# Performance work log

Hardware: AMD Instinct MI355X
Metric: run time of the kernel (lower is better)

Reference implementation:

```python
import jax, jax.numpy as jnp
import numpy as np

B, S, D, H, T = 64, 256, 256, 512, 48
EPS = 1e-5  # BatchNorm1d default eps


def setup_inputs():
    key = jax.random.key(0)
    ks = jax.random.split(key, 40)
    rn = lambda k, sh, s=0.05: jax.random.normal(k, sh, dtype=jnp.float32) * s
    inp = {}
    inp["inputs"] = jax.random.normal(ks[0], (B, S, D), dtype=jnp.float32)
    inp["tags"] = jax.random.randint(ks[1], (B, S), 0, T)
    i = 2
    for l, din in ((0, D), (1, 2 * H)):
        for d in ("f", "b"):
            inp["Wih_l%d%s" % (l, d)] = rn(ks[i], (4 * H, din)); i += 1
            inp["Whh_l%d%s" % (l, d)] = rn(ks[i], (4 * H, H)); i += 1
            inp["bih_l%d%s" % (l, d)] = rn(ks[i], (4 * H,)); i += 1
            inp["bhh_l%d%s" % (l, d)] = rn(ks[i], (4 * H,)); i += 1
    inp["bn_gamma"] = jnp.ones((2 * H,), jnp.float32)
    inp["bn_beta"] = jnp.zeros((2 * H,), jnp.float32)
    inp["bn_mean"] = rn(ks[i], (2 * H,)); i += 1
    inp["bn_var"] = jax.random.uniform(ks[i], (2 * H,), jnp.float32, 0.5, 1.5); i += 1
    inp["fc1_w"] = rn(ks[i], (H, 2 * H)); i += 1
    inp["fc1_b"] = rn(ks[i], (H,)); i += 1
    inp["fc2_w"] = rn(ks[i], (H // 2, H)); i += 1
    inp["fc2_b"] = rn(ks[i], (H // 2,)); i += 1
    inp["fc3_w"] = rn(ks[i], (T, H // 2)); i += 1
    inp["fc3_b"] = rn(ks[i], (T,)); i += 1
    inp["crf_start"] = rn(ks[i], (T,), 0.1); i += 1
    inp["crf_end"] = rn(ks[i], (T,), 0.1); i += 1
    inp["crf_trans"] = rn(ks[i], (T, T), 0.1); i += 1
    return inp


def _lstm_dir(x, Wih, Whh, bih, bhh, reverse):
    # x: [B,S,Din] -> hs: [B,S,H]; PyTorch gate order i,f,g,o
    xs = jnp.swapaxes(x, 0, 1)  # [S,B,Din]
    if reverse:
        xs = xs[::-1]
    pre = xs @ Wih.T + bih  # [S,B,4H] input projection precomputed
    h0 = jnp.zeros((x.shape[0], Whh.shape[1]), x.dtype)

    def step(carry, p):
        h, c = carry
        g = p + h @ Whh.T + bhh
        i, f, gg, o = jnp.split(g, 4, axis=-1)
        c = jax.nn.sigmoid(f) * c + jax.nn.sigmoid(i) * jnp.tanh(gg)
        h = jax.nn.sigmoid(o) * jnp.tanh(c)
        return (h, c), h

    _, hs = jax.lax.scan(step, (h0, h0), pre)
    if reverse:
        hs = hs[::-1]
    return jnp.swapaxes(hs, 0, 1)


def _model(inputs, tags, Wih_l0f, Whh_l0f, bih_l0f, bhh_l0f,
           Wih_l0b, Whh_l0b, bih_l0b, bhh_l0b,
           Wih_l1f, Whh_l1f, bih_l1f, bhh_l1f,
           Wih_l1b, Whh_l1b, bih_l1b, bhh_l1b,
           bn_gamma, bn_beta, bn_mean, bn_var,
           fc1_w, fc1_b, fc2_w, fc2_b, fc3_w, fc3_b,
           crf_start, crf_end, crf_trans):
    # 2-layer bidirectional LSTM
    x = jnp.concatenate([_lstm_dir(inputs, Wih_l0f, Whh_l0f, bih_l0f, bhh_l0f, False),
                         _lstm_dir(inputs, Wih_l0b, Whh_l0b, bih_l0b, bhh_l0b, True)], -1)
    x = jnp.concatenate([_lstm_dir(x, Wih_l1f, Whh_l1f, bih_l1f, bhh_l1f, False),
                         _lstm_dir(x, Wih_l1b, Whh_l1b, bih_l1b, bhh_l1b, True)], -1)
    # dropout: identity in eval; BatchNorm1d over channel dim, eval (running stats)
    x = (x - bn_mean) * (bn_gamma / jnp.sqrt(bn_var + EPS)) + bn_beta
    x = jax.nn.relu(x @ fc1_w.T + fc1_b)
    x = jax.nn.relu(x @ fc2_w.T + fc2_b)
    em = x @ fc3_w.T + fc3_b  # [B,S,T] emissions

    # CRF negative log-likelihood, full mask, reduction='mean'
    em_tag = jnp.take_along_axis(em, tags[..., None], axis=2)[..., 0]  # [B,S]
    num = (crf_start[tags[:, 0]] + em_tag.sum(1)
           + crf_trans[tags[:, :-1], tags[:, 1:]].sum(1)
           + crf_end[tags[:, -1]])

    et = jnp.swapaxes(em, 0, 1)  # [S,B,T]

    def step(alpha, e_t):
        # alpha: [B,T]; e_t: [B,T]
        alpha = jax.nn.logsumexp(alpha[:, :, None] + crf_trans[None], axis=1) + e_t
        return alpha, None

    alpha, _ = jax.lax.scan(step, crf_start + et[0], et[1:])
    logZ = jax.nn.logsumexp(alpha + crf_end, axis=1)
    return -jnp.mean(num - logZ)


def reference(inputs, tags, Wih_l0f, Whh_l0f, bih_l0f, bhh_l0f,
              Wih_l0b, Whh_l0b, bih_l0b, bhh_l0b,
              Wih_l1f, Whh_l1f, bih_l1f, bhh_l1f,
              Wih_l1b, Whh_l1b, bih_l1b, bhh_l1b,
              bn_gamma, bn_beta, bn_mean, bn_var,
              fc1_w, fc1_b, fc2_w, fc2_b, fc3_w, fc3_b,
              crf_start, crf_end, crf_trans):
    return _model(inputs, tags, Wih_l0f, Whh_l0f, bih_l0f, bhh_l0f,
                  Wih_l0b, Whh_l0b, bih_l0b, bhh_l0b,
                  Wih_l1f, Whh_l1f, bih_l1f, bhh_l1f,
                  Wih_l1b, Whh_l1b, bih_l1b, bhh_l1b,
                  bn_gamma, bn_beta, bn_mean, bn_var,
                  fc1_w, fc1_b, fc2_w, fc2_b, fc3_w, fc3_b,
                  crf_start, crf_end, crf_trans)
```

## Files before the change

kernel.cpp:

```cpp
#include <hip/hip_runtime.h>
#include <hip/hip_bf16.h>
#include <math.h>

#define Bz 64
#define Sz 256
#define Dz 256
#define Hz 512
#define FH 2048
#define OH 1024
#define Tz 48
#define EPSV 1e-5f
#define LOG2E 1.44269504f

typedef __hip_bfloat16 bf16;
typedef __attribute__((ext_vector_type(8))) short short8;
typedef __attribute__((ext_vector_type(4))) float floatx4;
typedef unsigned long long u64;

__device__ __forceinline__ float b2f(bf16 v){ return __bfloat162float(v); }
__device__ __forceinline__ float fsig(float x){
  float e = __builtin_amdgcn_exp2f(-x*LOG2E);
  return __builtin_amdgcn_rcpf(1.f + e);
}
__device__ __forceinline__ float ftanh(float x){
  float e = __builtin_amdgcn_exp2f(x*(2.f*LOG2E));
  return 1.f - 2.f*__builtin_amdgcn_rcpf(e + 1.f);
}

__device__ __forceinline__ void load4f(const bf16* p, float v[4]) {
  ushort4 t = *(const ushort4*)p;
  v[0] = __uint_as_float(((unsigned)t.x) << 16);
  v[1] = __uint_as_float(((unsigned)t.y) << 16);
  v[2] = __uint_as_float(((unsigned)t.z) << 16);
  v[3] = __uint_as_float(((unsigned)t.w) << 16);
}
__device__ __forceinline__ void storev(float* p, float v){ *p = v; }
__device__ __forceinline__ void storev(bf16* p, float v){ *p = __float2bfloat16(v); }

__global__ __launch_bounds__(256) void castf2b(const float* __restrict__ in, bf16* __restrict__ out, int n)
{
  int i = (blockIdx.x*256 + threadIdx.x)*4;
  if (i >= n) return;
  float4 v = *(const float4*)(in + i);
  bf16 tmp[4];
  tmp[0] = __float2bfloat16(v.x); tmp[1] = __float2bfloat16(v.y);
  tmp[2] = __float2bfloat16(v.z); tmp[3] = __float2bfloat16(v.w);
  *(uint2*)(out + i) = *(const uint2*)tmp;
}

__global__ __launch_bounds__(256) void bnprep_k(const float* __restrict__ gamma, const float* __restrict__ beta,
  const float* __restrict__ mean, const float* __restrict__ var,
  float* __restrict__ scale, float* __restrict__ shift)
{
  int i = blockIdx.x*256 + threadIdx.x;
  if (i >= OH) return;
  float s = gamma[i]*rsqrtf(var[i]+EPSV);
  scale[i] = s; shift[i] = beta[i] - mean[i]*s;
}

template<typename TC>
__global__ __launch_bounds__(256) void gemm_mfma(
  const bf16* __restrict__ A, const bf16* __restrict__ W,
  const float* __restrict__ b1, const float* __restrict__ b2,
  TC* __restrict__ Cv, int M, int N, int K, int relu)
{
  __shared__ bf16 As[128][40];
  __shared__ bf16 Bs[128][40];
  int tid = threadIdx.x;
  int wave = tid>>6, lane = tid&63, l15 = lane&15, quad = lane>>4;
  int m0 = blockIdx.y*128, n0 = blockIdx.x*128;
  int wm = (wave>>1)*64, wn = (wave&1)*64;
  int srow = tid>>1, scw = (tid&1)*16;
  const bf16* Ap = A + (size_t)(m0+srow)*K + scw;
  const bf16* Wp = W + (size_t)(n0+srow)*K + scw;
  floatx4 zero = {0.f,0.f,0.f,0.f};
  floatx4 acc[4][4];
  #pragma unroll
  for (int i=0;i<4;i++)
    #pragma unroll
    for (int j=0;j<4;j++) acc[i][j] = zero;

  for (int k0 = 0; k0 < K; k0 += 32) {
    float4 a0 = *(const float4*)Ap, a1 = *(const float4*)(Ap+8);
    float4 w0 = *(const float4*)Wp, w1 = *(const float4*)(Wp+8);
    Ap += 32; Wp += 32;
    __syncthreads();
    *(float4*)&As[srow][scw]   = a0; *(float4*)&As[srow][scw+8] = a1;
    *(float4*)&Bs[srow][scw]   = w0; *(float4*)&Bs[srow][scw+8] = w1;
    __syncthreads();
    short8 af[4], bfv[4];
    #pragma unroll
    for (int mi=0;mi<4;mi++) af[mi]  = *(const short8*)&As[wm+mi*16+l15][quad*8];
    #pragma unroll
    for (int ni=0;ni<4;ni++) bfv[ni] = *(const short8*)&Bs[wn+ni*16+l15][quad*8];
    #pragma unroll
    for (int mi=0;mi<4;mi++)
      #pragma unroll
      for (int ni=0;ni<4;ni++)
        acc[mi][ni] = __builtin_amdgcn_mfma_f32_16x16x32_bf16(af[mi], bfv[ni], acc[mi][ni], 0,0,0);
  }
  #pragma unroll
  for (int mi=0;mi<4;mi++){
    #pragma unroll
    for (int ni=0;ni<4;ni++){
      int n = n0 + wn + ni*16 + l15;
      float bb = (b1 ? b1[n] : 0.f) + (b2 ? b2[n] : 0.f);
      #pragma unroll
      for (int r=0;r<4;r++){
        int m = m0 + wm + mi*16 + quad*4 + r;
        float v = acc[mi][ni][r] + bb;
        if (relu) v = fmaxf(v, 0.f);
        storev(&Cv[(size_t)m*N + n], v);
      }
    }
  }
}

__global__ __launch_bounds__(256) void gemm_nt_small(
  const bf16* __restrict__ A, const float* __restrict__ W,
  const float* __restrict__ b1, float* __restrict__ Cv, int M, int N, int K)
{
  __shared__ float As[8][128];
  __shared__ float Ws[8][128];
  int tid = threadIdx.x;
  int tx = tid & 15, ty = tid >> 4;
  int m0 = blockIdx.y * 128, n0 = blockIdx.x * 128;
  int sr = tid >> 1;
  int sk = (tid & 1) * 4;
  const bf16* Ap = A + (size_t)(m0 + sr) * K + sk;
  bool wok = (n0 + sr) < N;
  const float* Wp = W + (size_t)(wok ? (n0 + sr) : 0) * K + sk;
  float acc[8][8] = {};
  for (int k0 = 0; k0 < K; k0 += 8) {
    float av[4], wv[4];
    load4f(Ap, av);
    if (wok) { float4 t = *(const float4*)Wp; wv[0]=t.x; wv[1]=t.y; wv[2]=t.z; wv[3]=t.w; }
    else { wv[0]=wv[1]=wv[2]=wv[3]=0.f; }
    Ap += 8; Wp += 8;
    __syncthreads();
    As[sk+0][sr]=av[0]; As[sk+1][sr]=av[1]; As[sk+2][sr]=av[2]; As[sk+3][sr]=av[3];
    Ws[sk+0][sr]=wv[0]; Ws[sk+1][sr]=wv[1]; Ws[sk+2][sr]=wv[2]; Ws[sk+3][sr]=wv[3];
    __syncthreads();
    #pragma unroll
    for (int kk = 0; kk < 8; kk++) {
      float a[8], w[8];
      *(float4*)&a[0] = *(const float4*)&As[kk][ty*8];
      *(float4*)&a[4] = *(const float4*)&As[kk][ty*8+4];
      *(float4*)&w[0] = *(const float4*)&Ws[kk][tx*8];
      *(float4*)&w[4] = *(const float4*)&Ws[kk][tx*8+4];
      #pragma unroll
      for (int i=0;i<8;i++)
        #pragma unroll
        for (int j=0;j<8;j++) acc[i][j] += a[i]*w[j];
    }
  }
  #pragma unroll
  for (int i=0;i<8;i++){
    int m = m0 + ty*8 + i;
    #pragma unroll
    for (int j=0;j<8;j++){
      int n = n0 + tx*8 + j;
      if (n < N) Cv[(size_t)m*N + n] = acc[i][j] + b1[n];
    }
  }
}

__global__ __launch_bounds__(256,1) void lstm_persist(
  const bf16* __restrict__ preF, const bf16* __restrict__ preB,
  const bf16* __restrict__ WF, const bf16* __restrict__ WB,
  bf16* __restrict__ hbuf,
  bf16* __restrict__ xout,
  const float* __restrict__ bnscale, const float* __restrict__ bnshift,
  int* __restrict__ cnt)
{
  __shared__ bf16 wlds[64][520];
  int blk = blockIdx.x;
  int dir = blk & 1;
  int js  = blk >> 1;
  int j0  = js * 16;
  const bf16* pre = dir ? preB : preF;
  const bf16* W   = dir ? WB : WF;
  int colOff = dir ? Hz : 0;
  int tid = threadIdx.x;
  int wave = tid >> 6, lane = tid & 63, l15 = lane & 15, quad = lane >> 4;
  int* myc = cnt + dir*256;

  for (int chunk = tid; chunk < 64*64; chunk += 256) {
    int n = chunk >> 6, col = (chunk & 63) * 8;
    int g = n >> 4, idx = n & 15;
    *(float4*)&wlds[n][col] = *(const float4*)(W + ((size_t)(g*512 + j0 + idx))*Hz + col);
  }
  __syncthreads();

  int bb = wave*16 + quad*4;
  int j  = j0 + l15;
  float sc = bnscale ? bnscale[colOff + j] : 1.f;
  float sh = bnshift ? bnshift[colOff + j] : 0.f;
  int useBN = bnscale ? 1 : 0;
  float c[4] = {0.f,0.f,0.f,0.f};

  float pg[4][4];
  {
    int t0 = dir ? (Sz-1) : 0;
    #pragma unroll
    for (int r=0;r<4;r++){
      const bf16* pb = pre + ((size_t)(bb+r)*Sz + t0)*FH;
      #pragma unroll
      for (int g=0;g<4;g++) pg[g][r] = b2f(pb[g*512 + j]);
    }
  }

  for (int t = 0; t < Sz; t++) {
    int tcur = dir ? (Sz-1-t) : t;
    floatx4 zero = {0.f,0.f,0.f,0.f};
    floatx4 acc[4] = {zero, zero, zero, zero};

    short8 af[16];
    if (t > 0) {
      const bf16* hprev = hbuf + ((size_t)((t&1)*2 + dir))*Bz*Hz;
      #pragma unroll
      for (int ks=0;ks<16;ks++){
        const u64* hp = (const u64*)(hprev + (size_t)(wave*16 + l15)*Hz + ks*32 + quad*8);
        union { u64 q[2]; short8 v; } uu;
        uu.q[0] = __hip_atomic_load(hp,     __ATOMIC_RELAXED, __HIP_MEMORY_SCOPE_SYSTEM);
        uu.q[1] = __hip_atomic_load(hp + 1, __ATOMIC_RELAXED, __HIP_MEMORY_SCOPE_SYSTEM);
        af[ks] = uu.v;
      }
    }

    float pgn[4][4];
    if (t+1 < Sz) {
      int tnext = dir ? (Sz-2-t) : (t+1);
      #pragma unroll
      for (int r=0;r<4;r++){
        const bf16* pb = pre + ((size_t)(bb+r)*Sz + tnext)*FH;
        #pragma unroll
        for (int g=0;g<4;g++) pgn[g][r] = b2f(pb[g*512 + j]);
      }
    }

    if (t > 0) {
      #pragma unroll
      for (int g=0; g<4; g++)
        #pragma unroll
        for (int ks=0; ks<16; ks++){
          short8 bfv = *(const short8*)&wlds[g*16 + l15][ks*32 + quad*8];
          acc[g] = __builtin_amdgcn_mfma_f32_16x16x32_bf16(af[ks], bfv, acc[g], 0,0,0);
        }
    }

    bf16* hnext = hbuf + ((size_t)(((t+1)&1)*2 + dir))*Bz*Hz;
    float hval[4];
    #pragma unroll
    for (int r=0;r<4;r++){
      int b = bb + r;
      float gi = acc[0][r] + pg[0][r];
      float gf = acc[1][r] + pg[1][r];
      float gg = acc[2][r] + pg[2][r];
      float go = acc[3][r] + pg[3][r];
      float cv = fsig(gf)*c[r] + fsig(gi)*ftanh(gg);
      float h  = fsig(go)*ftanh(cv);
      c[r] = cv;
      hval[r] = h;
      bf16 hb = __float2bfloat16(h);
      union { bf16 b16; short s; } u; u.b16 = hb;
      __hip_atomic_store((short*)(hnext + (size_t)b*Hz + j), u.s,
                         __ATOMIC_RELAXED, __HIP_MEMORY_SCOPE_SYSTEM);
    }

    if (t < Sz-1) {
      __syncthreads();
      if (tid == 0)
        __hip_atomic_fetch_add(&myc[t], 1, __ATOMIC_RELAXED, __HIP_MEMORY_SCOPE_SYSTEM);

      #pragma unroll
      for (int r=0;r<4;r++){
        float xv = useBN ? (hval[r]*sc + sh) : hval[r];
        xout[((size_t)(bb+r)*Sz + tcur)*OH + colOff + j] = __float2bfloat16(xv);
      }

      while (__hip_atomic_load(&myc[t], __ATOMIC_RELAXED, __HIP_MEMORY_SCOPE_SYSTEM) < 32) {}
      asm volatile("" ::: "memory");

      #pragma unroll
      for (int g=0;g<4;g++)
        #pragma unroll
        for (int r=0;r<4;r++) pg[g][r] = pgn[g][r];
    } else {
      #pragma unroll
      for (int r=0;r<4;r++){
        float xv = useBN ? (hval[r]*sc + sh) : hval[r];
        xout[((size_t)(bb+r)*Sz + tcur)*OH + colOff + j] = __float2bfloat16(xv);
      }
    }
  }
}

__global__ __launch_bounds__(64) void crf_k(const float* __restrict__ em, const int* __restrict__ tags,
  const float* __restrict__ start, const float* __restrict__ endv, const float* __restrict__ trans,
  float* __restrict__ result)
{
  __shared__ float tr[Tz*Tz];
  __shared__ float alpha[2][Tz];
  int b = blockIdx.x, tid = threadIdx.x;
  for (int i = tid; i < Tz*Tz; i += 64) tr[i] = trans[i];
  float np = 0.f;
  for (int t = tid; t < Sz; t += 64) {
    int tg = tags[b*Sz + t];
    np += em[((size_t)b*Sz + t)*Tz + tg];
    if (t+1 < Sz) np += trans[tg*Tz + tags[b*Sz + t + 1]];
  }
  #pragma unroll
  for (int off = 32; off; off >>= 1) np += __shfl_down(np, off);
  float num = 0.f;
  if (tid == 0) num = np + start[tags[b*Sz]] + endv[tags[b*Sz + Sz-1]];
  if (tid < Tz) alpha[0][tid] = start[tid] + em[((size_t)b*Sz)*Tz + tid];
  __syncthreads();
  int cur = 0;
  for (int t = 1; t < Sz; t++) {
    if (tid < Tz) {
      float m = -1e30f;
      for (int i = 0; i < Tz; i++) m = fmaxf(m, alpha[cur][i] + tr[i*Tz + tid]);
      float sum = 0.f;
      for (int i = 0; i < Tz; i++) sum += expf(alpha[cur][i] + tr[i*Tz + tid] - m);
      alpha[1-cur][tid] = m + logf(sum) + em[((size_t)b*Sz + t)*Tz + tid];
    }
    cur ^= 1;
    __syncthreads();
  }
  float a = (tid < Tz) ? alpha[cur][tid] + endv[tid] : -1e30f;
  float m = a;
  #pragma unroll
  for (int off = 32; off; off >>= 1) m = fmaxf(m, __shfl_down(m, off));
  m = __shfl(m, 0);
  float e = (tid < Tz) ? expf(a - m) : 0.f;
  #pragma unroll
  for (int off = 32; off; off >>= 1) e += __shfl_down(e, off);
  if (tid == 0) result[b] = num - (m + logf(e));
}

__global__ __launch_bounds__(64) void finalize_k(const float* __restrict__ result, float* __restrict__ outp)
{
  float v = result[threadIdx.x];
  #pragma unroll
  for (int off = 32; off; off >>= 1) v += __shfl_down(v, off);
  if (threadIdx.x == 0) outp[0] = -(v * (1.f/64.f));
}

extern "C" void kernel_launch(void* const* d_in, const int* in_sizes, int n_in,
                              void* d_out, int out_size, void* d_ws, size_t ws_size,
                              hipStream_t stream)
{
  (void)in_sizes; (void)n_in; (void)out_size; (void)ws_size;
  const float* inputs = (const float*)d_in[0];
  const int*   tags   = (const int*)d_in[1];
  const float* Wih[2][2] = {{(const float*)d_in[2],  (const float*)d_in[6]},
                            {(const float*)d_in[10], (const float*)d_in[14]}};
  const float* Whh[2][2] = {{(const float*)d_in[3],  (const float*)d_in[7]},
                            {(const float*)d_in[11], (const float*)d_in[15]}};
  const float* bih[2][2] = {{(const float*)d_in[4],  (const float*)d_in[8]},
                            {(const float*)d_in[12], (const float*)d_in[16]}};
  const float* bhh[2][2] = {{(const float*)d_in[5],  (const float*)d_in[9]},
                            {(const float*)d_in[13], (const float*)d_in[17]}};
  const float* bn_gamma = (const float*)d_in[18];
  const float* bn_beta  = (const float*)d_in[19];
  const float* bn_mean  = (const float*)d_in[20];
  const float* bn_var   = (const float*)d_in[21];
  const float* fc1_w = (const float*)d_in[22];
  const float* fc1_b = (const float*)d_in[23];
  const float* fc2_w = (const float*)d_in[24];
  const float* fc2_b = (const float*)d_in[25];
  const float* fc3_w = (const float*)d_in[26];
  const float* fc3_b = (const float*)d_in[27];
  const float* crf_start = (const float*)d_in[28];
  const float* crf_end   = (const float*)d_in[29];
  const float* crf_trans = (const float*)d_in[30];

  const size_t M = (size_t)Bz*Sz;
  char* p = (char*)d_ws;
  auto alloc = [&](size_t bytes) { char* r = p; p += (bytes + 255) & ~(size_t)255; return r; };
  bf16*  preF  = (bf16*) alloc(M*FH*sizeof(bf16));
  bf16*  preB  = (bf16*) alloc(M*FH*sizeof(bf16));
  bf16*  xbuf  = (bf16*) alloc(M*OH*sizeof(bf16));
  bf16*  inbf  = (bf16*) alloc(M*Dz*sizeof(bf16));
  bf16*  Wih0A = (bf16*) alloc((size_t)FH*Dz*sizeof(bf16));
  bf16*  Wih0B = (bf16*) alloc((size_t)FH*Dz*sizeof(bf16));
  bf16*  Wih1A = (bf16*) alloc((size_t)FH*OH*sizeof(bf16));
  bf16*  Wih1B = (bf16*) alloc((size_t)FH*OH*sizeof(bf16));
  bf16*  Whh0A = (bf16*) alloc((size_t)FH*Hz*sizeof(bf16));
  bf16*  Whh0B = (bf16*) alloc((size_t)FH*Hz*sizeof(bf16));
  bf16*  Whh1A = (bf16*) alloc((size_t)FH*Hz*sizeof(bf16));
  bf16*  Whh1B = (bf16*) alloc((size_t)FH*Hz*sizeof(bf16));
  bf16*  fc1wb = (bf16*) alloc((size_t)Hz*OH*sizeof(bf16));
  bf16*  fc2wb = (bf16*) alloc((size_t)256*Hz*sizeof(bf16));
  bf16*  hbuf  = (bf16*) alloc(4*(size_t)Bz*Hz*sizeof(bf16));
  int*   cnt   = (int*)  alloc(1024*sizeof(int));
  float* bnscale = (float*)alloc(OH*sizeof(float));
  float* bnshift = (float*)alloc(OH*sizeof(float));
  float* result  = (float*)alloc(Bz*sizeof(float));
  float* em   = (float*)inbf;
  bf16* fc1o = (bf16*)preF;
  bf16* fc2o = (bf16*)preB;

  dim3 tb(256);
  auto cast = [&](const float* src, bf16* dst, size_t n){
    castf2b<<<(n/4 + 255)/256, tb, 0, stream>>>(src, dst, (int)n);
  };

  hipMemsetAsync(cnt, 0, 1024*sizeof(int), stream);
  cast(inputs, inbf, M*Dz);
  cast(Wih[0][0], Wih0A, (size_t)FH*Dz);
  cast(Wih[0][1], Wih0B, (size_t)FH*Dz);
  cast(Wih[1][0], Wih1A, (size_t)FH*OH);
  cast(Wih[1][1], Wih1B, (size_t)FH*OH);
  cast(Whh[0][0], Whh0A, (size_t)FH*Hz);
  cast(Whh[0][1], Whh0B, (size_t)FH*Hz);
  cast(Whh[1][0], Whh1A, (size_t)FH*Hz);
  cast(Whh[1][1], Whh1B, (size_t)FH*Hz);
  cast(fc1_w, fc1wb, (size_t)Hz*OH);
  cast(fc2_w, fc2wb, (size_t)256*Hz);
  bnprep_k<<<OH/256, tb, 0, stream>>>(bn_gamma, bn_beta, bn_mean, bn_var, bnscale, bnshift);

  gemm_mfma<bf16><<<dim3(FH/128, M/128), tb, 0, stream>>>(inbf, Wih0A, bih[0][0], bhh[0][0], preF, M, FH, Dz, 0);
  gemm_mfma<bf16><<<dim3(FH/128, M/128), tb, 0, stream>>>(inbf, Wih0B, bih[0][1], bhh[0][1], preB, M, FH, Dz, 0);
  lstm_persist<<<64, tb, 0, stream>>>(preF, preB, Whh0A, Whh0B, hbuf, xbuf, nullptr, nullptr, cnt);
  gemm_mfma<bf16><<<dim3(FH/128, M/128), tb, 0, stream>>>(xbuf, Wih1A, bih[1][0], bhh[1][0], preF, M, FH, OH, 0);
  gemm_mfma<bf16><<<dim3(FH/128, M/128), tb, 0, stream>>>(xbuf, Wih1B, bih[1][1], bhh[1][1], preB, M, FH, OH, 0);
  lstm_persist<<<64, tb, 0, stream>>>(preF, preB, Whh1A, Whh1B, hbuf, xbuf, bnscale, bnshift, cnt + 512);
  gemm_mfma<bf16><<<dim3(Hz/128, M/128), tb, 0, stream>>>(xbuf, fc1wb, fc1_b, nullptr, fc1o, M, Hz, OH, 1);
  gemm_mfma<bf16><<<dim3(256/128, M/128), tb, 0, stream>>>(fc1o, fc2wb, fc2_b, nullptr, fc2o, M, 256, Hz, 1);
  gemm_nt_small<<<dim3(1, M/128), tb, 0, stream>>>(fc2o, fc3_w, fc3_b, em, M, Tz, 256);
  crf_k<<<Bz, 64, 0, stream>>>(em, tags, crf_start, crf_end, crf_trans, result);
  finalize_k<<<1, 64, 0, stream>>>(result, (float*)d_out);
}
```

Baseline: 4.417 ms.

## Replace atomic-counter grid barrier with per-block stamps and aggregator blocks

Each step's barrier in the persistent LSTM changes from 32 blocks doing atomic fetch-add on one counter per timestep to each block storing its own timestep stamp. Two extra aggregator blocks, one per direction, poll the 32 stamps with a wave-wide any test and publish an epoch value that the worker blocks spin on. This is meant to remove contention from atomic read-modify-writes on a shared counter and shorten the barrier latency on the sequential critical path. It adds an extra hop through the aggregator and depends on all 66 blocks being resident at the same time.

Result: slower. 4.685 ms (+6.1%).

```diff
diff --git a/kernel.cpp b/kernel.cpp
--- a/kernel.cpp
+++ b/kernel.cpp
@@ -171,10 +171,29 @@
   bf16* __restrict__ hbuf,
   bf16* __restrict__ xout,
   const float* __restrict__ bnscale, const float* __restrict__ bnshift,
-  int* __restrict__ cnt)
-{
+  int* __restrict__ flags)
+{
+  int blk = blockIdx.x;
+
+  if (blk >= 64) {
+    int dir = blk - 64;
+    if (threadIdx.x < 32) {
+      int* st = flags + dir*32;
+      int* ep = flags + 128 + dir*64;
+      int lane = threadIdx.x;
+      for (int t = 0; t < Sz-1; t++) {
+        int v;
+        do {
+          v = __hip_atomic_load(&st[lane], __ATOMIC_RELAXED, __HIP_MEMORY_SCOPE_SYSTEM);
+        } while (__any(v <= t));
+        if (lane == 0)
+          __hip_atomic_store(ep, t+1, __ATOMIC_RELAXED, __HIP_MEMORY_SCOPE_SYSTEM);
+      }
+    }
+    return;
+  }
+
   __shared__ bf16 wlds[64][520];
-  int blk = blockIdx.x;
   int dir = blk & 1;
   int js  = blk >> 1;
   int j0  = js * 16;
@@ -183,7 +202,8 @@
   int colOff = dir ? Hz : 0;
   int tid = threadIdx.x;
   int wave = tid >> 6, lane = tid & 63, l15 = lane & 15, quad = lane >> 4;
-  int* myc = cnt + dir*256;
+  int* mystamp = flags + dir*32 + js;
+  int* ep      = flags + 128 + dir*64;
 
   for (int chunk = tid; chunk < 64*64; chunk += 256) {
     int n = chunk >> 6, col = (chunk & 63) * 8;
@@ -271,7 +291,7 @@
     if (t < Sz-1) {
       __syncthreads();
       if (tid == 0)
-        __hip_atomic_fetch_add(&myc[t], 1, __ATOMIC_RELAXED, __HIP_MEMORY_SCOPE_SYSTEM);
+        __hip_atomic_store(mystamp, t+1, __ATOMIC_RELAXED, __HIP_MEMORY_SCOPE_SYSTEM);
 
       #pragma unroll
       for (int r=0;r<4;r++){
@@ -279,7 +299,7 @@
         xout[((size_t)(bb+r)*Sz + tcur)*OH + colOff + j] = __float2bfloat16(xv);
       }
 
-      while (__hip_atomic_load(&myc[t], __ATOMIC_RELAXED, __HIP_MEMORY_SCOPE_SYSTEM) < 32) {}
+      while (__hip_atomic_load(ep, __ATOMIC_RELAXED, __HIP_MEMORY_SCOPE_SYSTEM) <= t) {}
       asm volatile("" ::: "memory");
 
       #pragma unroll
@@ -394,7 +414,7 @@
   bf16*  fc1wb = (bf16*) alloc((size_t)Hz*OH*sizeof(bf16));
   bf16*  fc2wb = (bf16*) alloc((size_t)256*Hz*sizeof(bf16));
   bf16*  hbuf  = (bf16*) alloc(4*(size_t)Bz*Hz*sizeof(bf16));
-  int*   cnt   = (int*)  alloc(1024*sizeof(int));
+  int*   flags = (int*)  alloc(512*sizeof(int));
   float* bnscale = (float*)alloc(OH*sizeof(float));
   float* bnshift = (float*)alloc(OH*sizeof(float));
   float* result  = (float*)alloc(Bz*sizeof(float));
@@ -407,7 +427,7 @@
     castf2b<<<(n/4 + 255)/256, tb, 0, stream>>>(src, dst, (int)n);
   };
 
-  hipMemsetAsync(cnt, 0, 1024*sizeof(int), stream);
+  hipMemsetAsync(flags, 0, 512*sizeof(int), stream);
   cast(inputs, inbf, M*Dz);
   cast(Wih[0][0], Wih0A, (size_t)FH*Dz);
   cast(Wih[0][1], Wih0B, (size_t)FH*Dz);
@@ -423,10 +443,10 @@
 
   gemm_mfma<bf16><<<dim3(FH/128, M/128), tb, 0, stream>>>(inbf, Wih0A, bih[0][0], bhh[0][0], preF, M, FH, Dz, 0);
   gemm_mfma<bf16><<<dim3(FH/128, M/128), tb, 0, stream>>>(inbf, Wih0B, bih[0][1], bhh[0][1], preB, M, FH, Dz, 0);
-  lstm_persist<<<64, tb, 0, stream>>>(preF, preB, Whh0A, Whh0B, hbuf, xbuf, nullptr, nullptr, cnt);
+  lstm_persist<<<66, tb, 0, stream>>>(preF, preB, Whh0A, Whh0B, hbuf, xbuf, nullptr, nullptr, flags);
   gemm_mfma<bf16><<<dim3(FH/128, M/128), tb, 0, stream>>>(xbuf, Wih1A, bih[1][0], bhh[1][0], preF, M, FH, OH, 0);
   gemm_mfma<bf16><<<dim3(FH/128, M/128), tb, 0, stream>>>(xbuf, Wih1B, bih[1][1], bhh[1][1], preB, M, FH, OH, 0);
-  lstm_persist<<<64, tb, 0, stream>>>(preF, preB, Whh1A, Whh1B, hbuf, xbuf, bnscale, bnshift, cnt + 512);
+  lstm_persist<<<66, tb, 0, stream>>>(preF, preB, Whh1A, Whh1B, hbuf, xbuf, bnscale, bnshift, flags + 256);
   gemm_mfma<bf16><<<dim3(Hz/128, M/128), tb, 0, stream>>>(xbuf, fc1wb, fc1_b, nullptr, fc1o, M, Hz, OH, 1);
   gemm_mfma<bf16><<<dim3(256/128, M/128), tb, 0, stream>>>(fc1o, fc2wb, fc2_b, nullptr, fc2o, M, 256, Hz, 1);
   gemm_nt_small<<<dim3(1, M/128), tb, 0, stream>>>(fc2o, fc3_w, fc3_b, em, M, Tz, 256);
```

## Halve LSTM persistent blocks, each computing 32 hidden units per direction

Applied to the files above, without the earlier changes.

The persistent LSTM kernel now assigns 32 hidden columns per block instead of 16. That halves the grid to 32 blocks and the number of blocks participating in each per-timestep global barrier (16 per direction). Each block holds twice the recurrent weights in LDS (about 130KB) and does twice the MFMA work per step, reusing the loaded h fragments across both halves. The aim is to cut barrier and synchronisation latency on the serial recurrence, at the cost of more per-block compute and fewer CUs in use.

Result: slower. 5.214 ms (+18.1%).

```diff
diff --git a/kernel.cpp b/kernel.cpp
--- a/kernel.cpp
+++ b/kernel.cpp
@@ -173,11 +173,11 @@
   const float* __restrict__ bnscale, const float* __restrict__ bnshift,
   int* __restrict__ cnt)
 {
-  __shared__ bf16 wlds[64][520];
+  __shared__ bf16 wlds[128][520];
   int blk = blockIdx.x;
   int dir = blk & 1;
   int js  = blk >> 1;
-  int j0  = js * 16;
+  int j0  = js * 32;
   const bf16* pre = dir ? preB : preF;
   const bf16* W   = dir ? WB : WF;
   int colOff = dir ? Hz : 0;
@@ -185,35 +185,44 @@
   int wave = tid >> 6, lane = tid & 63, l15 = lane & 15, quad = lane >> 4;
   int* myc = cnt + dir*256;
 
-  for (int chunk = tid; chunk < 64*64; chunk += 256) {
+  for (int chunk = tid; chunk < 128*64; chunk += 256) {
     int n = chunk >> 6, col = (chunk & 63) * 8;
-    int g = n >> 4, idx = n & 15;
+    int g = n >> 5, idx = n & 31;
     *(float4*)&wlds[n][col] = *(const float4*)(W + ((size_t)(g*512 + j0 + idx))*Hz + col);
   }
   __syncthreads();
 
   int bb = wave*16 + quad*4;
-  int j  = j0 + l15;
-  float sc = bnscale ? bnscale[colOff + j] : 1.f;
-  float sh = bnshift ? bnshift[colOff + j] : 0.f;
+  float sc[2], sh[2];
+  #pragma unroll
+  for (int half=0; half<2; half++){
+    int j = j0 + half*16 + l15;
+    sc[half] = bnscale ? bnscale[colOff + j] : 1.f;
+    sh[half] = bnshift ? bnshift[colOff + j] : 0.f;
+  }
   int useBN = bnscale ? 1 : 0;
-  float c[4] = {0.f,0.f,0.f,0.f};
-
-  float pg[4][4];
+  float c[2][4] = {{0.f,0.f,0.f,0.f},{0.f,0.f,0.f,0.f}};
+
+  float pg[4][2][4];
   {
     int t0 = dir ? (Sz-1) : 0;
     #pragma unroll
     for (int r=0;r<4;r++){
       const bf16* pb = pre + ((size_t)(bb+r)*Sz + t0)*FH;
       #pragma unroll
-      for (int g=0;g<4;g++) pg[g][r] = b2f(pb[g*512 + j]);
+      for (int g=0;g<4;g++)
+        #pragma unroll
+        for (int half=0;half<2;half++)
+          pg[g][half][r] = b2f(pb[g*512 + j0 + half*16 + l15]);
     }
   }
 
   for (int t = 0; t < Sz; t++) {
     int tcur = dir ? (Sz-1-t) : t;
     floatx4 zero = {0.f,0.f,0.f,0.f};
-    floatx4 acc[4] = {zero, zero, zero, zero};
+    floatx4 acc[4][2];
+    #pragma unroll
+    for (int g=0;g<4;g++){ acc[g][0]=zero; acc[g][1]=zero; }
 
     short8 af[16];
     if (t > 0) {
@@ -228,14 +237,17 @@
       }
     }
 
-    float pgn[4][4];
+    float pgn[4][2][4];
     if (t+1 < Sz) {
       int tnext = dir ? (Sz-2-t) : (t+1);
       #pragma unroll
       for (int r=0;r<4;r++){
         const bf16* pb = pre + ((size_t)(bb+r)*Sz + tnext)*FH;
         #pragma unroll
-        for (int g=0;g<4;g++) pgn[g][r] = b2f(pb[g*512 + j]);
+        for (int g=0;g<4;g++)
+          #pragma unroll
+          for (int half=0;half<2;half++)
+            pgn[g][half][r] = b2f(pb[g*512 + j0 + half*16 + l15]);
       }
     }
 
@@ -243,29 +255,35 @@
       #pragma unroll
       for (int g=0; g<4; g++)
         #pragma unroll
-        for (int ks=0; ks<16; ks++){
-          short8 bfv = *(const short8*)&wlds[g*16 + l15][ks*32 + quad*8];
-          acc[g] = __builtin_amdgcn_mfma_f32_16x16x32_bf16(af[ks], bfv, acc[g], 0,0,0);
-        }
+        for (int half=0; half<2; half++)
+          #pragma unroll
+          for (int ks=0; ks<16; ks++){
+            short8 bfv = *(const short8*)&wlds[g*32 + half*16 + l15][ks*32 + quad*8];
+            acc[g][half] = __builtin_amdgcn_mfma_f32_16x16x32_bf16(af[ks], bfv, acc[g][half], 0,0,0);
+          }
     }
 
     bf16* hnext = hbuf + ((size_t)(((t+1)&1)*2 + dir))*Bz*Hz;
-    float hval[4];
-    #pragma unroll
-    for (int r=0;r<4;r++){
-      int b = bb + r;
-      float gi = acc[0][r] + pg[0][r];
-      float gf = acc[1][r] + pg[1][r];
-      float gg = acc[2][r] + pg[2][r];
-      float go = acc[3][r] + pg[3][r];
-      float cv = fsig(gf)*c[r] + fsig(gi)*ftanh(gg);
-      float h  = fsig(go)*ftanh(cv);
-      c[r] = cv;
-      hval[r] = h;
-      bf16 hb = __float2bfloat16(h);
-      union { bf16 b16; short s; } u; u.b16 = hb;
-      __hip_atomic_store((short*)(hnext + (size_t)b*Hz + j), u.s,
-                         __ATOMIC_RELAXED, __HIP_MEMORY_SCOPE_SYSTEM);
+    float hval[2][4];
+    #pragma unroll
+    for (int half=0; half<2; half++){
+      int j = j0 + half*16 + l15;
+      #pragma unroll
+      for (int r=0;r<4;r++){
+        int b = bb + r;
+        float gi = acc[0][half][r] + pg[0][half][r];
+        float gf = acc[1][half][r] + pg[1][half][r];
+        float gg = acc[2][half][r] + pg[2][half][r];
+        float go = acc[3][half][r] + pg[3][half][r];
+        float cv = fsig(gf)*c[half][r] + fsig(gi)*ftanh(gg);
+        float h  = fsig(go)*ftanh(cv);
+        c[half][r] = cv;
+        hval[half][r] = h;
+        bf16 hb = __float2bfloat16(h);
+        union { bf16 b16; short s; } u; u.b16 = hb;
+        __hip_atomic_store((short*)(hnext + (size_t)b*Hz + j), u.s,
+                           __ATOMIC_RELAXED, __HIP_MEMORY_SCOPE_SYSTEM);
+      }
     }
 
     if (t < Sz-1) {
@@ -274,23 +292,33 @@
         __hip_atomic_fetch_add(&myc[t], 1, __ATOMIC_RELAXED, __HIP_MEMORY_SCOPE_SYSTEM);
 
       #pragma unroll
-      for (int r=0;r<4;r++){
-        float xv = useBN ? (hval[r]*sc + sh) : hval[r];
-        xout[((size_t)(bb+r)*Sz + tcur)*OH + colOff + j] = __float2bfloat16(xv);
-      }
-
-      while (__hip_atomic_load(&myc[t], __ATOMIC_RELAXED, __HIP_MEMORY_SCOPE_SYSTEM) < 32) {}
+      for (int half=0; half<2; half++){
+        int j = j0 + half*16 + l15;
+        #pragma unroll
+        for (int r=0;r<4;r++){
+          float xv = useBN ? (hval[half][r]*sc[half] + sh[half]) : hval[half][r];
+          xout[((size_t)(bb+r)*Sz + tcur)*OH + colOff + j] = __float2bfloat16(xv);
+        }
+      }
+
+      while (__hip_atomic_load(&myc[t], __ATOMIC_RELAXED, __HIP_MEMORY_SCOPE_SYSTEM) < 16) {}
       asm volatile("" ::: "memory");
 
       #pragma unroll
       for (int g=0;g<4;g++)
         #pragma unroll
-        for (int r=0;r<4;r++) pg[g][r] = pgn[g][r];
+        for (int half=0;half<2;half++)
+          #pragma unroll
+          for (int r=0;r<4;r++) pg[g][half][r] = pgn[g][half][r];
     } else {
       #pragma unroll
-      for (int r=0;r<4;r++){
-        float xv = useBN ? (hval[r]*sc + sh) : hval[r];
-        xout[((size_t)(bb+r)*Sz + tcur)*OH + colOff + j] = __float2bfloat16(xv);
+      for (int half=0; half<2; half++){
+        int j = j0 + half*16 + l15;
+        #pragma unroll
+        for (int r=0;r<4;r++){
+          float xv = useBN ? (hval[half][r]*sc[half] + sh[half]) : hval[half][r];
+          xout[((size_t)(bb+r)*Sz + tcur)*OH + colOff + j] = __float2bfloat16(xv);
+        }
       }
     }
   }
@@ -423,10 +451,10 @@
 
   gemm_mfma<bf16><<<dim3(FH/128, M/128), tb, 0, stream>>>(inbf, Wih0A, bih[0][0], bhh[0][0], preF, M, FH, Dz, 0);
   gemm_mfma<bf16><<<dim3(FH/128, M/128), tb, 0, stream>>>(inbf, Wih0B, bih[0][1], bhh[0][1], preB, M, FH, Dz, 0);
-  lstm_persist<<<64, tb, 0, stream>>>(preF, preB, Whh0A, Whh0B, hbuf, xbuf, nullptr, nullptr, cnt);
+  lstm_persist<<<32, tb, 0, stream>>>(preF, preB, Whh0A, Whh0B, hbuf, xbuf, nullptr, nullptr, cnt);
   gemm_mfma<bf16><<<dim3(FH/128, M/128), tb, 0, stream>>>(xbuf, Wih1A, bih[1][0], bhh[1][0], preF, M, FH, OH, 0);
   gemm_mfma<bf16><<<dim3(FH/128, M/128), tb, 0, stream>>>(xbuf, Wih1B, bih[1][1], bhh[1][1], preB, M, FH, OH, 0);
-  lstm_persist<<<64, tb, 0, stream>>>(preF, preB, Whh1A, Whh1B, hbuf, xbuf, bnscale, bnshift, cnt + 512);
+  lstm_persist<<<32, tb, 0, stream>>>(preF, preB, Whh1A, Whh1B, hbuf, xbuf, bnscale, bnshift, cnt + 512);
   gemm_mfma<bf16><<<dim3(Hz/128, M/128), tb, 0, stream>>>(xbuf, fc1wb, fc1_b, nullptr, fc1o, M, Hz, OH, 1);
   gemm_mfma<bf16><<<dim3(256/128, M/128), tb, 0, stream>>>(fc1o, fc2wb, fc2_b, nullptr, fc2o, M, 256, Hz, 1);
   gemm_nt_small<<<dim3(1, M/128), tb, 0, stream>>>(fc2o, fc3_w, fc3_b, em, M, Tz, 256);
```
